# Kernel optimization log

Measured on AMD Instinct MI355X. Metric: run time of the kernel, lower is better.

The kernel has to match this reference:

```python
import jax, jax.numpy as jnp
import numpy as np

C = 1.0                 # ball curvature magnitude (k = -c)
SQRT_C = float(np.sqrt(C))
MIN_NORM = 1e-15
BALL_EPS = 4e-3         # geoopt float32 projection eps


def _artanh(x):
    return jnp.arctanh(jnp.clip(x, -1.0 + 1e-7, 1.0 - 1e-7))


def _norm(x):
    return jnp.clip(jnp.linalg.norm(x, axis=-1, keepdims=True), MIN_NORM)


def expmap0(u):
    n = _norm(u)
    return jnp.tanh(SQRT_C * n) * u / (SQRT_C * n)


def logmap0(y):
    n = _norm(y)
    return _artanh(SQRT_C * n) * y / (SQRT_C * n)


def mobius_add(x, y):
    x2 = jnp.sum(x * x, axis=-1, keepdims=True)
    y2 = jnp.sum(y * y, axis=-1, keepdims=True)
    xy = jnp.sum(x * y, axis=-1, keepdims=True)
    num = (1.0 + 2.0 * C * xy + C * y2) * x + (1.0 - C * x2) * y
    den = 1.0 + 2.0 * C * xy + C * C * x2 * y2
    return num / jnp.clip(den, MIN_NORM)


def mobius_matvec(W, x):
    # x: [N, in], W: [out, in]
    mx = x @ W.T                                   # [N, out]
    xn = _norm(x)
    mxn = _norm(mx)
    res = jnp.tanh(mxn / xn * _artanh(SQRT_C * xn)) * mx / (mxn * SQRT_C)
    zero = jnp.linalg.norm(mx, axis=-1, keepdims=True) <= 1e-10
    return jnp.where(zero, jnp.zeros_like(res), res)


def project(x):
    n = _norm(x)
    maxnorm = (1.0 - BALL_EPS) / SQRT_C
    return jnp.where(n > maxnorm, x * (maxnorm / n), x)


def setup_inputs() -> dict:
    key = jax.random.key(0)
    k1, k2, k3, k4, k5 = jax.random.split(key, 5)
    N, E, D_IN, D_OUT = 100000, 600000, 128, 128
    x_h = jax.random.normal(k1, (N, D_IN), dtype=jnp.float32) * 0.05  # inside ball
    edge_index = jax.random.randint(k2, (2, E), 0, N, dtype=jnp.int64)
    edge_weight = jax.random.uniform(k3, (E,), dtype=jnp.float32)
    xav = float(np.sqrt(2.0 / (D_IN + D_OUT)))
    W = jax.random.normal(k4, (D_OUT, D_IN), dtype=jnp.float32) * xav
    b = jax.random.normal(k5, (D_OUT,), dtype=jnp.float32) * 0.01
    a = jnp.asarray(0.25, dtype=jnp.float32)  # PReLU slope
    return {"x_h": x_h, "edge_index": edge_index, "edge_weight": edge_weight,
            "W": W, "b": b, "a": a}


def reference(x_h, edge_index, edge_weight, W, b, a):
    N = x_h.shape[0]
    # HyperbolicLinear: mobius matvec + mobius bias add
    h = mobius_matvec(W, x_h)
    h = mobius_add(h, expmap0(b))
    # tangent-space aggregation
    h_t = logmap0(h)                                  # [N, D]
    src, dst = edge_index[0], edge_index[1]
    msg = h_t[src] * edge_weight[:, None]             # [E, D]
    agg = jax.ops.segment_sum(msg, dst, num_segments=N) + h_t
    # mobius PReLU activation
    h2_t = logmap0(expmap0(agg))
    h2_t = jnp.where(h2_t >= 0, h2_t, a * h2_t)
    return project(expmap0(h2_t))
```

## Files before the change

kernel.cpp:

```cpp
#include <hip/hip_runtime.h>
#include <hip/hip_fp16.h>
#include <cstdint>

#define D 128
#define BLK 256

constexpr float MINN    = 1e-15f;
constexpr float ATCLIP  = 1.0f - 1e-7f;
constexpr float BALLEPS = 4e-3f;

typedef _Float16 f16x8 __attribute__((ext_vector_type(8)));
typedef float    f32x4 __attribute__((ext_vector_type(4)));

union H4 { _Float16 h[4]; uint2 u2; };
union H8 { _Float16 h[8]; uint4 u4; };

__device__ __forceinline__ float red64(float v) {
    v += __shfl_xor(v, 1, 64);
    v += __shfl_xor(v, 2, 64);
    v += __shfl_xor(v, 4, 64);
    v += __shfl_xor(v, 8, 64);
    v += __shfl_xor(v, 16, 64);
    v += __shfl_xor(v, 32, 64);
    return v;
}

__device__ __forceinline__ int red64i(int v) {
    v += __shfl_xor(v, 1, 64);
    v += __shfl_xor(v, 2, 64);
    v += __shfl_xor(v, 4, 64);
    v += __shfl_xor(v, 8, 64);
    v += __shfl_xor(v, 16, 64);
    v += __shfl_xor(v, 32, 64);
    return v;
}

__device__ __forceinline__ float red16(float v) {
    v += __shfl_xor(v, 1, 64);
    v += __shfl_xor(v, 2, 64);
    v += __shfl_xor(v, 4, 64);
    v += __shfl_xor(v, 8, 64);
    return v;
}

__device__ __forceinline__ float tanh_fast(float x) {
    float e = __expf(2.f * fminf(x, 15.f));
    return __fdividef(e - 1.f, e + 1.f);
}
__device__ __forceinline__ float artanh_fast(float x) {
    x = fminf(x, ATCLIP);
    return 0.5f * __logf(__fdividef(1.f + x, 1.f - x));
}

__global__ __launch_bounds__(256) void k_prep(const float* __restrict__ W,
                                              _Float16* __restrict__ Wh,
                                              int* __restrict__ zero, int zeroInts)
{
    const int t = threadIdx.x;
    const int bid = blockIdx.x;
    if (bid < 8) {
        int i = bid * 256 + t;
        int f = i >> 7;
        int r = i & 127;
        const float4* src = (const float4*)(W + r * 128 + f * 8);
        float4 v0 = src[0], v1 = src[1];
        H8 u;
        u.h[0] = (_Float16)v0.x; u.h[1] = (_Float16)v0.y;
        u.h[2] = (_Float16)v0.z; u.h[3] = (_Float16)v0.w;
        u.h[4] = (_Float16)v1.x; u.h[5] = (_Float16)v1.y;
        u.h[6] = (_Float16)v1.z; u.h[7] = (_Float16)v1.w;
        *(uint4*)(Wh + i * 8) = u.u4;
    } else {
        int i = (bid - 8) * 256 + t;
        int base = i * 4;
        if (base + 3 < zeroInts) {
            *(int4*)(zero + base) = make_int4(0, 0, 0, 0);
        } else if (base < zeroInts) {
            for (int k = base; k < zeroInts; ++k) zero[k] = 0;
        }
    }
}

__global__ __launch_bounds__(BLK) void k_node_mfma(
    const float* __restrict__ x, const _Float16* __restrict__ Wh,
    const float* __restrict__ b, uint2* __restrict__ ht, int N,
    const int* __restrict__ ei, int* __restrict__ cnt,
    int* __restrict__ rank, int E, int eslice, int use_rank)
{
    const int t     = threadIdx.x;
    const int node0 = blockIdx.x * 64;
    const int lane  = t & 63;
    const int w     = t >> 6;

    float2 b2 = ((const float2*)b)[lane];
    float pb  = fmaf(b2.x, b2.x, b2.y * b2.y);
    float bn2 = red64(pb);
    float bnc    = fmaxf(sqrtf(bn2), MINN);
    float bscale = __fdividef(tanh_fast(bnc), bnc);
    const float y2 = bscale * bscale * bn2;

    const int c = lane & 15;
    const int g = lane >> 4;
    const int bnode = w * 16 + c;
    const int gnode = node0 + bnode;
    const int gcl   = min(gnode, N - 1);
    const float* xrow = x + (size_t)gcl * 128;

    f32x4 xv[8];
#pragma unroll
    for (int s = 0; s < 4; ++s) {
        xv[2 * s]     = *(const f32x4*)&xrow[(s * 8 + g * 2) * 4];
        xv[2 * s + 1] = *(const f32x4*)&xrow[(s * 8 + g * 2 + 1) * 4];
    }

    float px = 0.f;
    f16x8 Bf[4];
#pragma unroll
    for (int s = 0; s < 4; ++s) {
        f32x4 lo = xv[2 * s], hi = xv[2 * s + 1];
        px = fmaf(lo[0], lo[0], px); px = fmaf(lo[1], lo[1], px);
        px = fmaf(lo[2], lo[2], px); px = fmaf(lo[3], lo[3], px);
        px = fmaf(hi[0], hi[0], px); px = fmaf(hi[1], hi[1], px);
        px = fmaf(hi[2], hi[2], px); px = fmaf(hi[3], hi[3], px);
        Bf[s][0] = (_Float16)lo[0]; Bf[s][1] = (_Float16)lo[1];
        Bf[s][2] = (_Float16)lo[2]; Bf[s][3] = (_Float16)lo[3];
        Bf[s][4] = (_Float16)hi[0]; Bf[s][5] = (_Float16)hi[1];
        Bf[s][6] = (_Float16)hi[2]; Bf[s][7] = (_Float16)hi[3];
    }

    f32x4 Cf[8];
#pragma unroll
    for (int mt = 0; mt < 8; ++mt) Cf[mt] = (f32x4){0.f, 0.f, 0.f, 0.f};

#pragma unroll
    for (int s = 0; s < 4; ++s) {
        const _Float16* wp = Wh + ((s * 4 + g) << 10) + (c << 3);
#pragma unroll
        for (int mt = 0; mt < 8; ++mt) {
            f16x8 Af = *(const f16x8*)&wp[mt << 7];
            Cf[mt] = __builtin_amdgcn_mfma_f32_16x16x32_f16(Af, Bf[s], Cf[mt], 0, 0, 0);
        }
    }

    const float4* b4 = (const float4*)b;
    float pm = 0.f, pdb = 0.f;
#pragma unroll
    for (int mt = 0; mt < 8; ++mt) {
        float4 bv = b4[mt * 4 + g];
        pm  = fmaf(Cf[mt][0], Cf[mt][0], pm);
        pm  = fmaf(Cf[mt][1], Cf[mt][1], pm);
        pm  = fmaf(Cf[mt][2], Cf[mt][2], pm);
        pm  = fmaf(Cf[mt][3], Cf[mt][3], pm);
        pdb = fmaf(Cf[mt][0], bv.x, pdb);
        pdb = fmaf(Cf[mt][1], bv.y, pdb);
        pdb = fmaf(Cf[mt][2], bv.z, pdb);
        pdb = fmaf(Cf[mt][3], bv.w, pdb);
    }
    float xn2 = px;
    xn2 += __shfl_xor(xn2, 16); xn2 += __shfl_xor(xn2, 32);
    pm  += __shfl_xor(pm, 16);  pm  += __shfl_xor(pm, 32);
    pdb += __shfl_xor(pdb, 16); pdb += __shfl_xor(pdb, 32);
    float pd = bscale * pdb;

    float xn      = fmaxf(sqrtf(xn2), MINN);
    float mxn_raw = sqrtf(pm);
    float mxn     = fmaxf(mxn_raw, MINN);
    float alpha   = __fdividef(tanh_fast(__fdividef(mxn, xn) * artanh_fast(xn)), mxn);
    if (mxn_raw <= 1e-10f) alpha = 0.f;

    float x2  = alpha * alpha * pm;
    float xy  = alpha * pd;
    float den = fmaxf(fmaf(x2, y2, 1.f + 2.f * xy), MINN);
    float ca  = __fdividef((1.f + 2.f * xy + y2) * alpha, den);
    float cb  = __fdividef(1.f - x2, den);

    float hn2 = ca * ca * pm + 2.f * ca * cb * pd + cb * cb * y2;
    float hn  = fmaxf(sqrtf(hn2), MINN);
    float lsc = __fdividef(artanh_fast(hn), hn);
    float s1  = lsc * ca;
    float s2b = lsc * cb * bscale;

    if (gnode < N) {
        uint2* orow = ht + (size_t)gnode * 32;
#pragma unroll
        for (int mt = 0; mt < 8; ++mt) {
            float4 bv = b4[mt * 4 + g];
            H4 u;
            u.h[0] = (_Float16)fmaf(s1, Cf[mt][0], s2b * bv.x);
            u.h[1] = (_Float16)fmaf(s1, Cf[mt][1], s2b * bv.y);
            u.h[2] = (_Float16)fmaf(s1, Cf[mt][2], s2b * bv.z);
            u.h[3] = (_Float16)fmaf(s1, Cf[mt][3], s2b * bv.w);
            orow[mt * 4 + g] = u.u2;
        }
    }

    {
        int e0 = blockIdx.x * eslice;
        if (use_rank) {
            for (int i = t; i < eslice; i += BLK) {
                int e = e0 + i;
                if (e < E) rank[e] = atomicAdd(&cnt[ei[E + e]], 1);
            }
        } else {
            for (int i = t; i < eslice; i += BLK) {
                int e = e0 + i;
                if (e < E) atomicAdd(&cnt[ei[E + e]], 1);
            }
        }
    }
}

__global__ __launch_bounds__(256) void k_scan(
    const int* __restrict__ cnt, int* __restrict__ ptr,
    unsigned long long* __restrict__ lb, int N)
{
    __shared__ int s[256];
    __shared__ int sbase;
    const int t   = threadIdx.x;
    const int bid = blockIdx.x;
    const int lane = t & 63;
    const int w    = t >> 6;

    int base = bid * 1024 + t * 4;
    int v0 = 0, v1 = 0, v2 = 0, v3 = 0;
    if (base + 3 < N) {
        int4 q = *(const int4*)&cnt[base];
        v0 = q.x; v1 = q.y; v2 = q.z; v3 = q.w;
    } else {
        if (base + 0 < N) v0 = cnt[base + 0];
        if (base + 1 < N) v1 = cnt[base + 1];
        if (base + 2 < N) v2 = cnt[base + 2];
        if (base + 3 < N) v3 = cnt[base + 3];
    }
    int sum = v0 + v1 + v2 + v3;
    s[t] = sum;
    __syncthreads();
    for (int off = 1; off < 256; off <<= 1) {
        int xv = (t >= off) ? s[t - off] : 0;
        __syncthreads();
        s[t] += xv;
        __syncthreads();
    }
    int excl  = s[t] - sum;
    int total = s[255];

    if (t == 255) {
        unsigned long long pkt =
            ((unsigned long long)((bid == 0) ? 2u : 1u) << 32) | (unsigned)total;
        __hip_atomic_store(&lb[bid], pkt, __ATOMIC_RELEASE, __HIP_MEMORY_SCOPE_AGENT);
        if (bid == 0) sbase = 0;
    }

    if (bid > 0 && w == 3) {
        int exclb = 0;
        int j = bid - 1;
        while (true) {
            int idx = j - lane;
            unsigned f = 0; int v = 0;
            if (idx >= 0) {
                unsigned long long p;
                do {
                    p = __hip_atomic_load(&lb[idx], __ATOMIC_ACQUIRE, __HIP_MEMORY_SCOPE_AGENT);
                    f = (unsigned)(p >> 32);
                } while (f == 0);
                v = (int)(unsigned)(p & 0xffffffffu);
            }
            unsigned long long m2 = __ballot(f == 2u);
            if (m2) {
                int Lstop = __ffsll((long long)m2) - 1;
                int contrib = (lane <= Lstop) ? v : 0;
                exclb += red64i(contrib);
                break;
            } else {
                exclb += red64i((idx >= 0) ? v : 0);
                j -= 64;
            }
        }
        if (lane == 0) {
            unsigned long long pkt2 =
                ((unsigned long long)2u << 32) | (unsigned)(exclb + total);
            __hip_atomic_store(&lb[bid], pkt2, __ATOMIC_RELEASE, __HIP_MEMORY_SCOPE_AGENT);
            sbase = exclb;
        }
    }
    __syncthreads();

    int r = excl + sbase;
    if (base + 0 < N) ptr[base + 0] = r; r += v0;
    if (base + 1 < N) ptr[base + 1] = r; r += v1;
    if (base + 2 < N) ptr[base + 2] = r; r += v2;
    if (base + 3 < N) ptr[base + 3] = r;
}

__global__ __launch_bounds__(256) void k_scatter_rank(
    const int* __restrict__ ei, const float* __restrict__ ew,
    const int* __restrict__ ptr, const int* __restrict__ rank,
    int2* __restrict__ sorted, int E)
{
    int e = blockIdx.x * 256 + threadIdx.x;
    if (e >= E) return;
    int src = ei[e];
    int dst = ei[E + e];
    float w = ew[e];
    int pos = ptr[dst] + rank[e];
    sorted[pos] = make_int2(src << 8, __float_as_int(w));
}

__global__ __launch_bounds__(256) void k_scatter_atomic(
    const int* __restrict__ ei, const float* __restrict__ ew,
    int* __restrict__ ptr, int2* __restrict__ sorted, int E)
{
    int e = blockIdx.x * 256 + threadIdx.x;
    if (e >= E) return;
    int src = ei[e];
    int dst = ei[E + e];
    float w = ew[e];
    int pos = atomicAdd(&ptr[dst], 1);
    sorted[pos] = make_int2(src << 8, __float_as_int(w));
}

__global__ __launch_bounds__(256) void k_agg_final(
    const char* __restrict__ htb, const int* __restrict__ ptr,
    const int* __restrict__ cnt, const int2* __restrict__ sorted,
    const float* __restrict__ a_in, float* __restrict__ out, int N, int rmode)
{
    const int t   = threadIdx.x;
    const int li  = t & 15;
    const int grp = t >> 4;
    const int n   = blockIdx.x * 16 + grp;
    if (n >= N) return;
    const float a = a_in[0];

    H8 own; own.u4 = *(const uint4*)(htb + (size_t)n * 256 + li * 16);
    float acc[8];
#pragma unroll
    for (int k = 0; k < 8; ++k) acc[k] = (float)own.h[k];

    int basep = ptr[n];
    int cn    = cnt[n];
    int s0    = rmode ? basep : basep - cn;
    int e0    = s0 + cn;

    const int lioff = li * 16;
    int j = s0;
    for (; j + 2 <= e0; j += 2) {
        int2 d0 = sorted[j];
        int2 d1 = sorted[j + 1];
        H8 g0, g1;
        g0.u4 = *(const uint4*)(htb + (unsigned)d0.x + lioff);
        g1.u4 = *(const uint4*)(htb + (unsigned)d1.x + lioff);
        float w0 = __int_as_float(d0.y);
        float w1 = __int_as_float(d1.y);
#pragma unroll
        for (int k = 0; k < 8; ++k) acc[k] = fmaf((float)g0.h[k], w0, acc[k]);
#pragma unroll
        for (int k = 0; k < 8; ++k) acc[k] = fmaf((float)g1.h[k], w1, acc[k]);
    }
    if (j < e0) {
        int2 d = sorted[j];
        H8 g; g.u4 = *(const uint4*)(htb + (unsigned)d.x + lioff);
        float w = __int_as_float(d.y);
#pragma unroll
        for (int k = 0; k < 8; ++k) acc[k] = fmaf((float)g.h[k], w, acc[k]);
    }

    float pv = 0.f;
#pragma unroll
    for (int k = 0; k < 8; ++k) {
        float v = acc[k];
        v = (v >= 0.f) ? v : a * v;
        acc[k] = v;
        pv = fmaf(v, v, pv);
    }
    float m2 = red16(pv);
    float rc = fmaxf(sqrtf(m2), MINN);
    float te = tanh_fast(rc);
    const float maxn = 1.0f - BALLEPS;
    float fsc = __fdividef(fminf(fmaxf(te, MINN), maxn), rc);

    float4 o0 = make_float4(fsc * acc[0], fsc * acc[1], fsc * acc[2], fsc * acc[3]);
    float4 o1 = make_float4(fsc * acc[4], fsc * acc[5], fsc * acc[6], fsc * acc[7]);
    float4* orow = (float4*)(out + (size_t)n * D);
    orow[li * 2 + 0] = o0;
    orow[li * 2 + 1] = o1;
}

extern "C" void kernel_launch(void* const* d_in, const int* in_sizes, int n_in,
                              void* d_out, int out_size, void* d_ws, size_t ws_size,
                              hipStream_t stream)
{
    const float* x  = (const float*)d_in[0];
    const int*   ei = (const int*)  d_in[1];
    const float* ew = (const float*)d_in[2];
    const float* W  = (const float*)d_in[3];
    const float* b  = (const float*)d_in[4];
    const float* a  = (const float*)d_in[5];
    float* out = (float*)d_out;

    const int N = in_sizes[0] / D;
    const int E = in_sizes[1] / 2;
    const int nc = (N + 1023) / 1024;

    char* ws = (char*)d_ws;
    size_t HT_B       = (size_t)N * D * 2;
    uint2*              ht  = (uint2*)ws;
    size_t off_cnt    = HT_B;
    int*                cnt = (int*)(ws + off_cnt);
    size_t off_lb     = (off_cnt + (size_t)N * 4 + 15) & ~(size_t)15;
    unsigned long long* lb  = (unsigned long long*)(ws + off_lb);
    size_t off_ptr    = (off_lb + (size_t)nc * 8 + 15) & ~(size_t)15;
    int*                ptr = (int*)(ws + off_ptr);
    size_t off_sorted = (off_ptr + (size_t)N * 4 + 15) & ~(size_t)15;
    int2*               sorted = (int2*)(ws + off_sorted);
    size_t off_wh     = off_sorted + (size_t)E * 8;
    _Float16*           Wh  = (_Float16*)(ws + off_wh);
    size_t off_rank   = off_wh + 32768;
    int*                rank = (int*)(ws + off_rank);
    int use_rank = (ws_size >= off_rank + (size_t)E * 4) ? 1 : 0;

    int zeroInts = (int)((off_ptr - off_cnt) / 4);
    int zb  = ((zeroInts + 3) / 4 + 255) / 256;
    int nb1 = (N + 63) / 64;
    int eslice = (E + nb1 - 1) / nb1;

    k_prep<<<8 + zb, 256, 0, stream>>>(W, Wh, cnt, zeroInts);
    k_node_mfma<<<nb1, BLK, 0, stream>>>(x, Wh, b, ht, N, ei, cnt,
                                         use_rank ? rank : nullptr, E, eslice, use_rank);
    k_scan<<<nc, 256, 0, stream>>>(cnt, ptr, lb, N);
    if (use_rank)
        k_scatter_rank<<<(E + 255) / 256, 256, 0, stream>>>(ei, ew, ptr, rank, sorted, E);
    else
        k_scatter_atomic<<<(E + 255) / 256, 256, 0, stream>>>(ei, ew, ptr, sorted, E);
    k_agg_final<<<(N + 15) / 16, 256, 0, stream>>>((const char*)ht, ptr, cnt, sorted, a, out, N, use_rank);
}
```

Baseline: 200.0 us.

## Split edge histogram into own kernel and pipeline node GEMM through LDS

Moves the destination-degree histogram and rank atomics out of the node MFMA kernel into a separate vectorized k_hist kernel. The node kernel now handles 128 nodes per block: it loads the first 64 rows into swizzled LDS with global_load_lds and the next 64 into registers at the same time. It also stages outputs through LDS so the ht writes are coalesced. The aggregation loop is unrolled from 2 to 4 edges for more memory-level parallelism, at the cost of an extra kernel launch, more LDS and register pressure, and fewer blocks in flight.

```diff
diff --git a/kernel.cpp b/kernel.cpp
--- a/kernel.cpp
+++ b/kernel.cpp
@@ -14,6 +14,9 @@
 
 union H4 { _Float16 h[4]; uint2 u2; };
 union H8 { _Float16 h[8]; uint4 u4; };
+
+typedef __attribute__((address_space(1))) const void gas_v;
+typedef __attribute__((address_space(3))) void las_v;
 
 __device__ __forceinline__ float red64(float v) {
     v += __shfl_xor(v, 1, 64);
@@ -81,18 +84,65 @@
     }
 }
 
+__global__ __launch_bounds__(256) void k_hist(const int* __restrict__ ei,
+                                              int* __restrict__ cnt,
+                                              int* __restrict__ rank,
+                                              int E, int use_rank)
+{
+    const int* dsts = ei + E;
+    int i0 = (blockIdx.x * 256 + threadIdx.x) * 4;
+    if (((E & 3) == 0) && (i0 + 4 <= E)) {
+        int4 d = *(const int4*)(dsts + i0);
+        int r0 = atomicAdd(&cnt[d.x], 1);
+        int r1 = atomicAdd(&cnt[d.y], 1);
+        int r2 = atomicAdd(&cnt[d.z], 1);
+        int r3 = atomicAdd(&cnt[d.w], 1);
+        if (use_rank) *(int4*)(rank + i0) = make_int4(r0, r1, r2, r3);
+    } else {
+        for (int e = i0; e < E && e < i0 + 4; ++e) {
+            int r = atomicAdd(&cnt[dsts[e]], 1);
+            if (use_rank) rank[e] = r;
+        }
+    }
+}
+
 __global__ __launch_bounds__(BLK) void k_node_mfma(
     const float* __restrict__ x, const _Float16* __restrict__ Wh,
-    const float* __restrict__ b, uint2* __restrict__ ht, int N,
-    const int* __restrict__ ei, int* __restrict__ cnt,
-    int* __restrict__ rank, int E, int eslice, int use_rank)
-{
+    const float* __restrict__ b, uint2* __restrict__ ht, int N)
+{
+    __shared__ float xs[64 * 128];
+
     const int t     = threadIdx.x;
-    const int node0 = blockIdx.x * 64;
     const int lane  = t & 63;
     const int w     = t >> 6;
+    const int node0 = blockIdx.x * 128;
 
     float2 b2 = ((const float2*)b)[lane];
+    __builtin_amdgcn_sched_barrier(0);
+
+#pragma unroll
+    for (int i = 0; i < 8; ++i) {
+        int P      = (w * 8 + i) * 64 + lane;
+        int node   = P >> 5;
+        int q      = (P & 31) ^ (node & 7);
+        int node_g = min(node0 + node, N - 1);
+        const float* src = x + (size_t)node_g * 128 + q * 4;
+        char* dst = (char*)xs + (size_t)(w * 8 + i) * 1024;
+        __builtin_amdgcn_global_load_lds((gas_v*)src, (las_v*)dst, 16, 0, 0);
+    }
+    __builtin_amdgcn_sched_barrier(0);
+
+    f32x4 rv[8];
+#pragma unroll
+    for (int i = 0; i < 8; ++i) {
+        int P      = (w * 8 + i) * 64 + lane;
+        int node   = P >> 5;
+        int q      = (P & 31) ^ (node & 7);
+        int node_g = min(node0 + 64 + node, N - 1);
+        rv[i] = *(const f32x4*)(x + (size_t)node_g * 128 + q * 4);
+    }
+    __builtin_amdgcn_sched_barrier(0);
+
     float pb  = fmaf(b2.x, b2.x, b2.y * b2.y);
     float bn2 = red64(pb);
     float bnc    = fmaxf(sqrtf(bn2), MINN);
@@ -102,86 +152,76 @@
     const int c = lane & 15;
     const int g = lane >> 4;
     const int bnode = w * 16 + c;
-    const int gnode = node0 + bnode;
-    const int gcl   = min(gnode, N - 1);
-    const float* xrow = x + (size_t)gcl * 128;
-
-    f32x4 xv[8];
-#pragma unroll
-    for (int s = 0; s < 4; ++s) {
-        xv[2 * s]     = *(const f32x4*)&xrow[(s * 8 + g * 2) * 4];
-        xv[2 * s + 1] = *(const f32x4*)&xrow[(s * 8 + g * 2 + 1) * 4];
-    }
-
-    float px = 0.f;
-    f16x8 Bf[4];
-#pragma unroll
-    for (int s = 0; s < 4; ++s) {
-        f32x4 lo = xv[2 * s], hi = xv[2 * s + 1];
-        px = fmaf(lo[0], lo[0], px); px = fmaf(lo[1], lo[1], px);
-        px = fmaf(lo[2], lo[2], px); px = fmaf(lo[3], lo[3], px);
-        px = fmaf(hi[0], hi[0], px); px = fmaf(hi[1], hi[1], px);
-        px = fmaf(hi[2], hi[2], px); px = fmaf(hi[3], hi[3], px);
-        Bf[s][0] = (_Float16)lo[0]; Bf[s][1] = (_Float16)lo[1];
-        Bf[s][2] = (_Float16)lo[2]; Bf[s][3] = (_Float16)lo[3];
-        Bf[s][4] = (_Float16)hi[0]; Bf[s][5] = (_Float16)hi[1];
-        Bf[s][6] = (_Float16)hi[2]; Bf[s][7] = (_Float16)hi[3];
-    }
-
-    f32x4 Cf[8];
-#pragma unroll
-    for (int mt = 0; mt < 8; ++mt) Cf[mt] = (f32x4){0.f, 0.f, 0.f, 0.f};
-
-#pragma unroll
-    for (int s = 0; s < 4; ++s) {
-        const _Float16* wp = Wh + ((s * 4 + g) << 10) + (c << 3);
+    const int sw    = bnode & 7;
+    const float* xrow = &xs[bnode * 128];
+    const float4* b4  = (const float4*)b;
+    uint2* lout = (uint2*)((char*)xs + (size_t)w * 8192);
+
+    auto do_tile = [&](int tb) {
+        f32x4 Cf[8];
+#pragma unroll
+        for (int mt = 0; mt < 8; ++mt) Cf[mt] = (f32x4){0.f, 0.f, 0.f, 0.f};
+        float px = 0.f;
+
+#pragma unroll
+        for (int s = 0; s < 4; ++s) {
+            int q0 = s * 8 + g * 2;
+            f32x4 lo = *(const f32x4*)&xrow[(q0 ^ sw) * 4];
+            f32x4 hi = *(const f32x4*)&xrow[((q0 + 1) ^ sw) * 4];
+            px = fmaf(lo[0], lo[0], px); px = fmaf(lo[1], lo[1], px);
+            px = fmaf(lo[2], lo[2], px); px = fmaf(lo[3], lo[3], px);
+            px = fmaf(hi[0], hi[0], px); px = fmaf(hi[1], hi[1], px);
+            px = fmaf(hi[2], hi[2], px); px = fmaf(hi[3], hi[3], px);
+            f16x8 Bf;
+            Bf[0] = (_Float16)lo[0]; Bf[1] = (_Float16)lo[1];
+            Bf[2] = (_Float16)lo[2]; Bf[3] = (_Float16)lo[3];
+            Bf[4] = (_Float16)hi[0]; Bf[5] = (_Float16)hi[1];
+            Bf[6] = (_Float16)hi[2]; Bf[7] = (_Float16)hi[3];
+            const _Float16* wp = Wh + ((s * 4 + g) << 10) + (c << 3);
+#pragma unroll
+            for (int mt = 0; mt < 8; ++mt) {
+                f16x8 Af = *(const f16x8*)&wp[mt << 7];
+                Cf[mt] = __builtin_amdgcn_mfma_f32_16x16x32_f16(Af, Bf, Cf[mt], 0, 0, 0);
+            }
+        }
+
+        float pm = 0.f, pdb = 0.f;
 #pragma unroll
         for (int mt = 0; mt < 8; ++mt) {
-            f16x8 Af = *(const f16x8*)&wp[mt << 7];
-            Cf[mt] = __builtin_amdgcn_mfma_f32_16x16x32_f16(Af, Bf[s], Cf[mt], 0, 0, 0);
-        }
-    }
-
-    const float4* b4 = (const float4*)b;
-    float pm = 0.f, pdb = 0.f;
-#pragma unroll
-    for (int mt = 0; mt < 8; ++mt) {
-        float4 bv = b4[mt * 4 + g];
-        pm  = fmaf(Cf[mt][0], Cf[mt][0], pm);
-        pm  = fmaf(Cf[mt][1], Cf[mt][1], pm);
-        pm  = fmaf(Cf[mt][2], Cf[mt][2], pm);
-        pm  = fmaf(Cf[mt][3], Cf[mt][3], pm);
-        pdb = fmaf(Cf[mt][0], bv.x, pdb);
-        pdb = fmaf(Cf[mt][1], bv.y, pdb);
-        pdb = fmaf(Cf[mt][2], bv.z, pdb);
-        pdb = fmaf(Cf[mt][3], bv.w, pdb);
-    }
-    float xn2 = px;
-    xn2 += __shfl_xor(xn2, 16); xn2 += __shfl_xor(xn2, 32);
-    pm  += __shfl_xor(pm, 16);  pm  += __shfl_xor(pm, 32);
-    pdb += __shfl_xor(pdb, 16); pdb += __shfl_xor(pdb, 32);
-    float pd = bscale * pdb;
-
-    float xn      = fmaxf(sqrtf(xn2), MINN);
-    float mxn_raw = sqrtf(pm);
-    float mxn     = fmaxf(mxn_raw, MINN);
-    float alpha   = __fdividef(tanh_fast(__fdividef(mxn, xn) * artanh_fast(xn)), mxn);
-    if (mxn_raw <= 1e-10f) alpha = 0.f;
-
-    float x2  = alpha * alpha * pm;
-    float xy  = alpha * pd;
-    float den = fmaxf(fmaf(x2, y2, 1.f + 2.f * xy), MINN);
-    float ca  = __fdividef((1.f + 2.f * xy + y2) * alpha, den);
-    float cb  = __fdividef(1.f - x2, den);
-
-    float hn2 = ca * ca * pm + 2.f * ca * cb * pd + cb * cb * y2;
-    float hn  = fmaxf(sqrtf(hn2), MINN);
-    float lsc = __fdividef(artanh_fast(hn), hn);
-    float s1  = lsc * ca;
-    float s2b = lsc * cb * bscale;
-
-    if (gnode < N) {
-        uint2* orow = ht + (size_t)gnode * 32;
+            float4 bv = b4[mt * 4 + g];
+            pm  = fmaf(Cf[mt][0], Cf[mt][0], pm);
+            pm  = fmaf(Cf[mt][1], Cf[mt][1], pm);
+            pm  = fmaf(Cf[mt][2], Cf[mt][2], pm);
+            pm  = fmaf(Cf[mt][3], Cf[mt][3], pm);
+            pdb = fmaf(Cf[mt][0], bv.x, pdb);
+            pdb = fmaf(Cf[mt][1], bv.y, pdb);
+            pdb = fmaf(Cf[mt][2], bv.z, pdb);
+            pdb = fmaf(Cf[mt][3], bv.w, pdb);
+        }
+        float xn2 = px;
+        xn2 += __shfl_xor(xn2, 16); xn2 += __shfl_xor(xn2, 32);
+        pm  += __shfl_xor(pm, 16);  pm  += __shfl_xor(pm, 32);
+        pdb += __shfl_xor(pdb, 16); pdb += __shfl_xor(pdb, 32);
+        float pd = bscale * pdb;
+
+        float xn      = fmaxf(sqrtf(xn2), MINN);
+        float mxn_raw = sqrtf(pm);
+        float mxn     = fmaxf(mxn_raw, MINN);
+        float alpha   = __fdividef(tanh_fast(__fdividef(mxn, xn) * artanh_fast(xn)), mxn);
+        if (mxn_raw <= 1e-10f) alpha = 0.f;
+
+        float x2  = alpha * alpha * pm;
+        float xy  = alpha * pd;
+        float den = fmaxf(fmaf(x2, y2, 1.f + 2.f * xy), MINN);
+        float ca  = __fdividef((1.f + 2.f * xy + y2) * alpha, den);
+        float cb  = __fdividef(1.f - x2, den);
+
+        float hn2 = ca * ca * pm + 2.f * ca * cb * pd + cb * cb * y2;
+        float hn  = fmaxf(sqrtf(hn2), MINN);
+        float lsc = __fdividef(artanh_fast(hn), hn);
+        float s1  = lsc * ca;
+        float s2b = lsc * cb * bscale;
+
 #pragma unroll
         for (int mt = 0; mt < 8; ++mt) {
             float4 bv = b4[mt * 4 + g];
@@ -190,24 +230,45 @@
             u.h[1] = (_Float16)fmaf(s1, Cf[mt][1], s2b * bv.y);
             u.h[2] = (_Float16)fmaf(s1, Cf[mt][2], s2b * bv.z);
             u.h[3] = (_Float16)fmaf(s1, Cf[mt][3], s2b * bv.w);
-            orow[mt * 4 + g] = u.u2;
-        }
-    }
-
-    {
-        int e0 = blockIdx.x * eslice;
-        if (use_rank) {
-            for (int i = t; i < eslice; i += BLK) {
-                int e = e0 + i;
-                if (e < E) rank[e] = atomicAdd(&cnt[ei[E + e]], 1);
+            lout[c * 33 + mt * 4 + g] = u.u2;
+        }
+    };
+
+    auto copyout = [&](int tb) {
+#pragma unroll
+        for (int it = 0; it < 8; ++it) {
+            int lin  = it * BLK + t;
+            int node = lin >> 5;
+            int col  = lin & 31;
+            int gn   = tb + node;
+            if (gn < N) {
+                const uint2* lsrc = (const uint2*)((const char*)xs + (size_t)(node >> 4) * 8192);
+                ht[(size_t)gn * 32 + col] = lsrc[(node & 15) * 33 + col];
             }
-        } else {
-            for (int i = t; i < eslice; i += BLK) {
-                int e = e0 + i;
-                if (e < E) atomicAdd(&cnt[ei[E + e]], 1);
-            }
-        }
-    }
+        }
+    };
+
+    asm volatile("s_waitcnt vmcnt(8)" ::: "memory");
+    __builtin_amdgcn_sched_barrier(0);
+
+    do_tile(node0);
+    __syncthreads();
+    copyout(node0);
+
+    asm volatile("s_waitcnt lgkmcnt(0)" ::: "memory");
+    __builtin_amdgcn_sched_barrier(0);
+    __builtin_amdgcn_s_barrier();
+    __builtin_amdgcn_sched_barrier(0);
+
+#pragma unroll
+    for (int i = 0; i < 8; ++i) {
+        float* dst = (float*)((char*)xs + (size_t)(w * 8 + i) * 1024 + (size_t)lane * 16);
+        *(f32x4*)dst = rv[i];
+    }
+
+    do_tile(node0 + 64);
+    __syncthreads();
+    copyout(node0 + 64);
 }
 
 __global__ __launch_bounds__(256) void k_scan(
@@ -343,20 +404,30 @@
 
     const int lioff = li * 16;
     int j = s0;
-    for (; j + 2 <= e0; j += 2) {
+    for (; j + 4 <= e0; j += 4) {
         int2 d0 = sorted[j];
         int2 d1 = sorted[j + 1];
-        H8 g0, g1;
+        int2 d2 = sorted[j + 2];
+        int2 d3 = sorted[j + 3];
+        H8 g0, g1, g2, g3;
         g0.u4 = *(const uint4*)(htb + (unsigned)d0.x + lioff);
         g1.u4 = *(const uint4*)(htb + (unsigned)d1.x + lioff);
+        g2.u4 = *(const uint4*)(htb + (unsigned)d2.x + lioff);
+        g3.u4 = *(const uint4*)(htb + (unsigned)d3.x + lioff);
         float w0 = __int_as_float(d0.y);
         float w1 = __int_as_float(d1.y);
+        float w2 = __int_as_float(d2.y);
+        float w3 = __int_as_float(d3.y);
 #pragma unroll
         for (int k = 0; k < 8; ++k) acc[k] = fmaf((float)g0.h[k], w0, acc[k]);
 #pragma unroll
         for (int k = 0; k < 8; ++k) acc[k] = fmaf((float)g1.h[k], w1, acc[k]);
-    }
-    if (j < e0) {
+#pragma unroll
+        for (int k = 0; k < 8; ++k) acc[k] = fmaf((float)g2.h[k], w2, acc[k]);
+#pragma unroll
+        for (int k = 0; k < 8; ++k) acc[k] = fmaf((float)g3.h[k], w3, acc[k]);
+    }
+    for (; j < e0; ++j) {
         int2 d = sorted[j];
         H8 g; g.u4 = *(const uint4*)(htb + (unsigned)d.x + lioff);
         float w = __int_as_float(d.y);
@@ -420,12 +491,12 @@
 
     int zeroInts = (int)((off_ptr - off_cnt) / 4);
     int zb  = ((zeroInts + 3) / 4 + 255) / 256;
-    int nb1 = (N + 63) / 64;
-    int eslice = (E + nb1 - 1) / nb1;
+    int nb1 = (N + 127) / 128;
+    int hb  = (E + 1023) / 1024;
 
     k_prep<<<8 + zb, 256, 0, stream>>>(W, Wh, cnt, zeroInts);
-    k_node_mfma<<<nb1, BLK, 0, stream>>>(x, Wh, b, ht, N, ei, cnt,
-                                         use_rank ? rank : nullptr, E, eslice, use_rank);
+    k_hist<<<hb, 256, 0, stream>>>(ei, cnt, use_rank ? rank : cnt, E, use_rank);
+    k_node_mfma<<<nb1, BLK, 0, stream>>>(x, Wh, b, ht, N);
     k_scan<<<nc, 256, 0, stream>>>(cnt, ptr, lb, N);
     if (use_rank)
         k_scatter_rank<<<(E + 255) / 256, 256, 0, stream>>>(ei, ew, ptr, rank, sorted, E);
```

New measurement: 212.0 us. 6.0% more time.
